# Optimization experiments

Hardware: AMD Instinct MI355X
Metric: run time of the kernel (lower is better)

Reference implementation:

```python
import jax, jax.numpy as jnp
import numpy as np

DIM = 512
NUM_HEADS = 8
HEAD_DIM = DIM // NUM_HEADS
B, N = 2, 4096


def setup_inputs() -> dict:
    key = jax.random.key(0)
    k1, k2, k3, k4, k5 = jax.random.split(key, 5)
    s = 1.0 / np.sqrt(DIM)
    return {
        "x": jax.random.normal(k1, (B, N, DIM), dtype=jnp.float32),
        "w_qkv": jax.random.normal(k2, (DIM, 3 * DIM), dtype=jnp.float32) * s,
        "b_qkv": jax.random.normal(k3, (3 * DIM,), dtype=jnp.float32) * 0.01,
        "w_proj": jax.random.normal(k4, (DIM, DIM), dtype=jnp.float32) * s,
        "b_proj": jax.random.normal(k5, (DIM,), dtype=jnp.float32) * 0.01,
    }


def reference(x, w_qkv, b_qkv, w_proj, b_proj):
    b, n, c = x.shape
    h, d = NUM_HEADS, HEAD_DIM
    qkv = x @ w_qkv + b_qkv                      # [B,N,3C]
    q, k, v = jnp.split(qkv, 3, axis=-1)
    # [B,N,C] -> [B,H,N,D]
    q = q.reshape(b, n, h, d).transpose(0, 2, 1, 3)
    k = k.reshape(b, n, h, d).transpose(0, 2, 1, 3)
    v = v.reshape(b, n, h, d).transpose(0, 2, 1, 3)
    scale = d ** (-0.5)
    attn = jnp.einsum('bhqd,bhkd->bhqk', q, k) * scale  # [B,H,N,N]
    attn = jax.nn.softmax(attn, axis=-1)
    out = jnp.einsum('bhqk,bhkd->bhqd', attn, v)        # [B,H,N,D]
    out = out.transpose(0, 2, 1, 3).reshape(b, n, c)
    return out @ w_proj + b_proj
```

## Files before the change

### kernel.cpp

```cpp
#include <hip/hip_runtime.h>

#define DIM_C 512
#define HEADS 8
#define HD 64
#define BATCH 2
#define SEQ 4096
#define QSCALE (0.125f * 1.44269504088896f)

typedef __attribute__((ext_vector_type(8))) short short8;
typedef __attribute__((ext_vector_type(4))) float f32x4;

__device__ __forceinline__ ushort f2bf(float f) {
    union { float f; unsigned u; } x; x.f = f;
    unsigned r = x.u + 0x7fffu + ((x.u >> 16) & 1u);
    return (ushort)(r >> 16);
}

__device__ __forceinline__ void gl_lds16(const void* g, void* l) {
    __builtin_amdgcn_global_load_lds(
        (const __attribute__((address_space(1))) unsigned int*)g,
        (__attribute__((address_space(3))) unsigned int*)l, 16, 0, 0);
}

__device__ __forceinline__ unsigned cvt_pk_bf16(float lo, float hi) {
    unsigned w;
    asm("v_cvt_pk_bf16_f32 %0, %1, %2" : "=v"(w) : "v"(lo), "v"(hi));
    return w;
}

__global__ __launch_bounds__(256)
void convert_bf16(const float* __restrict__ in, ushort* __restrict__ out, int n4) {
    int i = blockIdx.x * blockDim.x + threadIdx.x;
    const int stride = gridDim.x * blockDim.x;
    for (; i < n4; i += stride) {
        const float4 v = reinterpret_cast<const float4*>(in)[i];
        ushort4 o;
        o.x = f2bf(v.x); o.y = f2bf(v.y); o.z = f2bf(v.z); o.w = f2bf(v.w);
        reinterpret_cast<ushort4*>(out)[i] = o;
    }
}

__global__ __launch_bounds__(256)
void transpose_w_bf16(const float* __restrict__ in, ushort* __restrict__ out,
                      int R, int C) {
    __shared__ ushort Ls[64 * 68];
    const int tid = threadIdx.x;
    const int c0 = blockIdx.x * 64, r0 = blockIdx.y * 64;
    #pragma unroll
    for (int p = 0; p < 4; ++p) {
        const int idx = tid + p * 256;
        const int r = idx >> 4, c4 = (idx & 15) * 4;
        const float4 v = *reinterpret_cast<const float4*>(
            &in[(size_t)(r0 + r) * C + c0 + c4]);
        ushort4 o; o.x = f2bf(v.x); o.y = f2bf(v.y); o.z = f2bf(v.z); o.w = f2bf(v.w);
        *reinterpret_cast<ushort4*>(&Ls[r * 68 + c4]) = o;
    }
    __syncthreads();
    #pragma unroll
    for (int p = 0; p < 4; ++p) {
        const int idx = tid + p * 256;
        const int c = idx >> 4, r4 = (idx & 15) * 4;
        ushort4 o;
        o.x = Ls[(r4 + 0) * 68 + c]; o.y = Ls[(r4 + 1) * 68 + c];
        o.z = Ls[(r4 + 2) * 68 + c]; o.w = Ls[(r4 + 3) * 68 + c];
        *reinterpret_cast<ushort4*>(&out[(size_t)(c0 + c) * R + r0 + r4]) = o;
    }
}

__global__ __launch_bounds__(256)
void transpose_v(const ushort* __restrict__ qkvb, ushort* __restrict__ vt) {
    __shared__ ushort Ls[64 * 68];
    const int tid = threadIdx.x;
    const int n0 = blockIdx.x * 64;
    const int bh = blockIdx.y, b = bh >> 3, h = bh & 7;
    #pragma unroll
    for (int p = 0; p < 4; ++p) {
        const int idx = tid + p * 256;
        const int r = idx >> 4, c4 = (idx & 15) * 4;
        const ushort4 v = *reinterpret_cast<const ushort4*>(
            &qkvb[(size_t)(b * SEQ + n0 + r) * 1536 + 1024 + h * 64 + c4]);
        *reinterpret_cast<ushort4*>(&Ls[r * 68 + c4]) = v;
    }
    __syncthreads();
    #pragma unroll
    for (int p = 0; p < 4; ++p) {
        const int idx = tid + p * 256;
        const int d = idx >> 4, n4 = (idx & 15) * 4;
        ushort4 o;
        o.x = Ls[(n4 + 0) * 68 + d]; o.y = Ls[(n4 + 1) * 68 + d];
        o.z = Ls[(n4 + 2) * 68 + d]; o.w = Ls[(n4 + 3) * 68 + d];
        *reinterpret_cast<ushort4*>(&vt[((size_t)bh * 64 + d) * SEQ + n0 + n4]) = o;
    }
}

template<int MODE>
__global__ __launch_bounds__(256)
void gemm_mfma(const ushort* __restrict__ A, const ushort* __restrict__ BT,
               const float* __restrict__ bias, void* __restrict__ Cout,
               int M, int N, int K) {
    __shared__ ushort As[128 * 64];
    __shared__ ushort Bs[128 * 64];
    const int tid = threadIdx.x;
    const int lane = tid & 63, wid = tid >> 6;
    const int lr = lane & 15, lg = lane >> 4;
    const int wm = wid >> 1, wn = wid & 1;
    const int rowBase = blockIdx.y * 128, colBase = blockIdx.x * 128;
    const int l8 = lane >> 3;
    const int lchunk = (lane & 7) ^ l8;

    f32x4 acc[4][4];
    #pragma unroll
    for (int i = 0; i < 4; ++i)
        #pragma unroll
        for (int j = 0; j < 4; ++j)
            #pragma unroll
            for (int c = 0; c < 4; ++c) acc[i][j][c] = 0.f;

    for (int k0 = 0; k0 < K; k0 += 64) {
        #pragma unroll
        for (int i = 0; i < 4; ++i) {
            const int r = wid * 32 + i * 8;
            gl_lds16(&A[(size_t)(rowBase + r + l8) * K + k0 + lchunk * 8],
                     &As[r * 64]);
            gl_lds16(&BT[(size_t)(colBase + r + l8) * K + k0 + lchunk * 8],
                     &Bs[r * 64]);
        }
        __syncthreads();
        #pragma unroll
        for (int s = 0; s < 2; ++s) {
            short8 af[4], bf[4];
            #pragma unroll
            for (int mt = 0; mt < 4; ++mt) {
                const int r = wm * 64 + mt * 16 + lr;
                af[mt] = *reinterpret_cast<const short8*>(
                    &As[r * 64 + ((s * 4 + lg) ^ (r & 7)) * 8]);
            }
            #pragma unroll
            for (int nt = 0; nt < 4; ++nt) {
                const int r = wn * 64 + nt * 16 + lr;
                bf[nt] = *reinterpret_cast<const short8*>(
                    &Bs[r * 64 + ((s * 4 + lg) ^ (r & 7)) * 8]);
            }
            #pragma unroll
            for (int mt = 0; mt < 4; ++mt)
                #pragma unroll
                for (int nt = 0; nt < 4; ++nt)
                    acc[mt][nt] = __builtin_amdgcn_mfma_f32_16x16x32_bf16(
                        bf[nt], af[mt], acc[mt][nt], 0, 0, 0);
        }
        __syncthreads();
    }

    #pragma unroll
    for (int nt = 0; nt < 4; ++nt) {
        const int c0 = colBase + wn * 64 + nt * 16 + lg * 4;
        const float4 bv = *reinterpret_cast<const float4*>(&bias[c0]);
        const float qs = (MODE == 1 && c0 < DIM_C) ? QSCALE : 1.f;
        #pragma unroll
        for (int mt = 0; mt < 4; ++mt) {
            const int row = rowBase + wm * 64 + mt * 16 + lr;
            if (MODE == 0) {
                float4 o;
                o.x = acc[mt][nt][0] + bv.x; o.y = acc[mt][nt][1] + bv.y;
                o.z = acc[mt][nt][2] + bv.z; o.w = acc[mt][nt][3] + bv.w;
                *reinterpret_cast<float4*>(
                    &reinterpret_cast<float*>(Cout)[(size_t)row * N + c0]) = o;
            } else {
                uint2 o;
                o.x = cvt_pk_bf16((acc[mt][nt][0] + bv.x) * qs,
                                  (acc[mt][nt][1] + bv.y) * qs);
                o.y = cvt_pk_bf16((acc[mt][nt][2] + bv.z) * qs,
                                  (acc[mt][nt][3] + bv.w) * qs);
                *reinterpret_cast<uint2*>(
                    &reinterpret_cast<ushort*>(Cout)[(size_t)row * N + c0]) = o;
            }
        }
    }
}

__global__ __launch_bounds__(512)
void flash_attn7(const ushort* __restrict__ qkvb, const ushort* __restrict__ vt,
                 ushort* __restrict__ aoutb) {
    __shared__ ushort Ks[2][64 * 64];
    __shared__ ushort Vs[2][64 * 64];
    __shared__ ushort Ps[8 * 16 * 64];

    const int tid = threadIdx.x;
    const int lane = tid & 63, wid = tid >> 6;
    const int lr = lane & 15, lg = lane >> 4;
    const int qt = blockIdx.x, bh = blockIdx.y;
    const int b = bh >> 3, h = bh & 7;
    const int q0 = qt * 128;
    const int l8 = lane >> 3;
    const int lchunk = (lane & 7) ^ l8;
    const int rsw = (lr & 7) ^ ((lr >> 3) << 2);

    short8 onesf;
    #pragma unroll
    for (int i = 0; i < 8; ++i) onesf[i] = (short)0x3F80;

    short8 qf[2];
    {
        const size_t qrow = (size_t)b * SEQ + q0 + wid * 16 + lr;
        #pragma unroll
        for (int s = 0; s < 2; ++s)
            qf[s] = *reinterpret_cast<const short8*>(
                &qkvb[qrow * 1536 + h * 64 + s * 32 + lg * 8]);
    }

    float m = -1e30f;
    f32x4 lacc;
    lacc[0] = 0.f; lacc[1] = 0.f; lacc[2] = 0.f; lacc[3] = 0.f;
    f32x4 oa[4];
    #pragma unroll
    for (int dt = 0; dt < 4; ++dt)
        #pragma unroll
        for (int c = 0; c < 4; ++c) oa[dt][c] = 0.f;

    auto stage = [&](int kt, int buf) {
        const int k0 = kt * 64;
        const int r = wid * 8;
        gl_lds16(&qkvb[(size_t)(b * SEQ + k0 + r + l8) * 1536 + DIM_C +
                       h * 64 + lchunk * 8],
                 &Ks[buf][r * 64]);
        gl_lds16(&vt[((size_t)bh * 64 + r + l8) * SEQ + k0 + lchunk * 8],
                 &Vs[buf][r * 64]);
    };

    stage(0, 0);
    const int NT = SEQ / 64;
    for (int kt = 0; kt < NT; ++kt) {
        const int buf = kt & 1;
        __syncthreads();
        if (kt + 1 < NT) stage(kt + 1, buf ^ 1);

        f32x4 sa[4];
        #pragma unroll
        for (int t = 0; t < 4; ++t)
            #pragma unroll
            for (int c = 0; c < 4; ++c) sa[t][c] = 0.f;
        __builtin_amdgcn_s_setprio(1);
        #pragma unroll
        for (int t = 0; t < 4; ++t) {
            const int n = t * 16 + lr;
            #pragma unroll
            for (int s = 0; s < 2; ++s) {
                const short8 kf = *reinterpret_cast<const short8*>(
                    &Ks[buf][n * 64 + ((s * 4 + lg) ^ (n & 7)) * 8]);
                sa[t] = __builtin_amdgcn_mfma_f32_16x16x32_bf16(
                    kf, qf[s], sa[t], 0, 0, 0);
            }
        }
        __builtin_amdgcn_s_setprio(0);

        float mx = fmaxf(fmaxf(sa[0][0], sa[0][1]), sa[0][2]);
        mx = fmaxf(fmaxf(mx, sa[0][3]), sa[1][0]);
        mx = fmaxf(fmaxf(mx, sa[1][1]), sa[1][2]);
        mx = fmaxf(fmaxf(mx, sa[1][3]), sa[2][0]);
        mx = fmaxf(fmaxf(mx, sa[2][1]), sa[2][2]);
        mx = fmaxf(fmaxf(mx, sa[2][3]), sa[3][0]);
        mx = fmaxf(fmaxf(mx, sa[3][1]), sa[3][2]);
        mx = fmaxf(mx, sa[3][3]);
        mx = fmaxf(mx, __shfl_xor(mx, 16));
        mx = fmaxf(mx, __shfl_xor(mx, 32));
        if (__any(mx > m + 8.f)) {
            const float mnew = fmaxf(m, mx);
            const float alpha = exp2f(m - mnew);
            m = mnew;
            lacc[0] *= alpha; lacc[1] *= alpha;
            lacc[2] *= alpha; lacc[3] *= alpha;
            const float a0 = __shfl(alpha, lg * 4 + 0);
            const float a1 = __shfl(alpha, lg * 4 + 1);
            const float a2 = __shfl(alpha, lg * 4 + 2);
            const float a3 = __shfl(alpha, lg * 4 + 3);
            #pragma unroll
            for (int dt = 0; dt < 4; ++dt) {
                oa[dt][0] *= a0; oa[dt][1] *= a1;
                oa[dt][2] *= a2; oa[dt][3] *= a3;
            }
        }
        #pragma unroll
        for (int t = 0; t < 4; ++t)
            #pragma unroll
            for (int r = 0; r < 4; ++r)
                sa[t][r] = exp2f(sa[t][r] - m);

        const int pb = wid * (16 * 64);
        const int pbase = pb + lr * 64 + (lg & 1) * 4;
        #pragma unroll
        for (int t = 0; t < 4; ++t) {
            const int chunk = (2 * t + (lg >> 1)) ^ rsw;
            uint2 w;
            w.x = cvt_pk_bf16(sa[t][0], sa[t][1]);
            w.y = cvt_pk_bf16(sa[t][2], sa[t][3]);
            *reinterpret_cast<uint2*>(&Ps[pbase + chunk * 8]) = w;
        }

        short8 pf[2];
        #pragma unroll
        for (int s = 0; s < 2; ++s)
            pf[s] = *reinterpret_cast<const short8*>(
                &Ps[pb + lr * 64 + ((lg + 4 * s) ^ rsw) * 8]);

        __builtin_amdgcn_s_setprio(1);
        #pragma unroll
        for (int s = 0; s < 2; ++s)
            lacc = __builtin_amdgcn_mfma_f32_16x16x32_bf16(
                onesf, pf[s], lacc, 0, 0, 0);
        #pragma unroll
        for (int dt = 0; dt < 4; ++dt) {
            const int d = dt * 16 + lr;
            #pragma unroll
            for (int s = 0; s < 2; ++s) {
                const short8 vf = *reinterpret_cast<const short8*>(
                    &Vs[buf][d * 64 + ((s * 4 + lg) ^ (d & 7)) * 8]);
                oa[dt] = __builtin_amdgcn_mfma_f32_16x16x32_bf16(
                    pf[s], vf, oa[dt], 0, 0, 0);
            }
        }
        __builtin_amdgcn_s_setprio(0);
    }

    const float linv = 1.f / lacc[0];
    const float v0 = __shfl(linv, lg * 4 + 0);
    const float v1 = __shfl(linv, lg * 4 + 1);
    const float v2 = __shfl(linv, lg * 4 + 2);
    const float v3 = __shfl(linv, lg * 4 + 3);
    const size_t orow0 = (size_t)b * SEQ + q0 + wid * 16;
    #pragma unroll
    for (int dt = 0; dt < 4; ++dt) {
        const int c = h * HD + dt * 16 + lr;
        aoutb[(orow0 + lg * 4 + 0) * DIM_C + c] = f2bf(oa[dt][0] * v0);
        aoutb[(orow0 + lg * 4 + 1) * DIM_C + c] = f2bf(oa[dt][1] * v1);
        aoutb[(orow0 + lg * 4 + 2) * DIM_C + c] = f2bf(oa[dt][2] * v2);
        aoutb[(orow0 + lg * 4 + 3) * DIM_C + c] = f2bf(oa[dt][3] * v3);
    }
}

extern "C" void kernel_launch(void* const* d_in, const int* in_sizes, int n_in,
                              void* d_out, int out_size, void* d_ws, size_t ws_size,
                              hipStream_t stream) {
    const float* x      = (const float*)d_in[0];
    const float* w_qkv  = (const float*)d_in[1];
    const float* b_qkv  = (const float*)d_in[2];
    const float* w_proj = (const float*)d_in[3];
    const float* b_proj = (const float*)d_in[4];
    float* out = (float*)d_out;

    const int M = BATCH * SEQ;
    ushort* xb     = (ushort*)d_ws;
    ushort* wqkvT  = xb     + (size_t)M * DIM_C;
    ushort* wprojT = wqkvT  + (size_t)3 * DIM_C * DIM_C;
    ushort* qkvb   = wprojT + (size_t)DIM_C * DIM_C;
    ushort* vt     = qkvb   + (size_t)M * 3 * DIM_C;
    ushort* aoutb  = vt     + (size_t)16 * HD * SEQ;

    convert_bf16<<<2048, 256, 0, stream>>>(x, xb, M * DIM_C / 4);
    transpose_w_bf16<<<dim3(3 * DIM_C / 64, DIM_C / 64), 256, 0, stream>>>(
        w_qkv, wqkvT, DIM_C, 3 * DIM_C);
    transpose_w_bf16<<<dim3(DIM_C / 64, DIM_C / 64), 256, 0, stream>>>(
        w_proj, wprojT, DIM_C, DIM_C);

    gemm_mfma<1><<<dim3(3 * DIM_C / 128, M / 128), 256, 0, stream>>>(
        xb, wqkvT, b_qkv, qkvb, M, 3 * DIM_C, DIM_C);

    transpose_v<<<dim3(SEQ / 64, BATCH * HEADS), 256, 0, stream>>>(qkvb, vt);

    flash_attn7<<<dim3(SEQ / 128, BATCH * HEADS), 512, 0, stream>>>(
        qkvb, vt, aoutb);

    gemm_mfma<0><<<dim3(DIM_C / 128, M / 128), 256, 0, stream>>>(
        aoutb, wprojT, b_proj, out, M, DIM_C, DIM_C);
}
```

Baseline: 251.2 us.

## Double attention key tile to 128 and switch GEMM epilogue to scalar stores

The flash-attention kernel now stages 128 keys per iteration instead of 64. It computes eight score tiles per step and processes the P·V product in two 64-key halves, which halves the loop trip count, barriers and online-softmax max checks. The GEMM swaps its MFMA operand order so the accumulator layout changes, and its epilogue now writes per-element scalar stores with a scalar bias load instead of vector float4/uint2 stores. The larger tile raises LDS use and register pressure, and the scalar epilogue may coalesce worse than the vector stores.

After: 243.0 us. 3.3% less time.

```diff
diff --git a/kernel.cpp b/kernel.cpp
--- a/kernel.cpp
+++ b/kernel.cpp
@@ -146,43 +146,36 @@
                 #pragma unroll
                 for (int nt = 0; nt < 4; ++nt)
                     acc[mt][nt] = __builtin_amdgcn_mfma_f32_16x16x32_bf16(
-                        bf[nt], af[mt], acc[mt][nt], 0, 0, 0);
+                        af[mt], bf[nt], acc[mt][nt], 0, 0, 0);
         }
         __syncthreads();
     }
 
     #pragma unroll
     for (int nt = 0; nt < 4; ++nt) {
-        const int c0 = colBase + wn * 64 + nt * 16 + lg * 4;
-        const float4 bv = *reinterpret_cast<const float4*>(&bias[c0]);
-        const float qs = (MODE == 1 && c0 < DIM_C) ? QSCALE : 1.f;
+        const int col = colBase + wn * 64 + nt * 16 + lr;
+        const float bv = bias[col];
+        const float qs = (MODE == 1 && col < DIM_C) ? QSCALE : 1.f;
         #pragma unroll
         for (int mt = 0; mt < 4; ++mt) {
-            const int row = rowBase + wm * 64 + mt * 16 + lr;
-            if (MODE == 0) {
-                float4 o;
-                o.x = acc[mt][nt][0] + bv.x; o.y = acc[mt][nt][1] + bv.y;
-                o.z = acc[mt][nt][2] + bv.z; o.w = acc[mt][nt][3] + bv.w;
-                *reinterpret_cast<float4*>(
-                    &reinterpret_cast<float*>(Cout)[(size_t)row * N + c0]) = o;
-            } else {
-                uint2 o;
-                o.x = cvt_pk_bf16((acc[mt][nt][0] + bv.x) * qs,
-                                  (acc[mt][nt][1] + bv.y) * qs);
-                o.y = cvt_pk_bf16((acc[mt][nt][2] + bv.z) * qs,
-                                  (acc[mt][nt][3] + bv.w) * qs);
-                *reinterpret_cast<uint2*>(
-                    &reinterpret_cast<ushort*>(Cout)[(size_t)row * N + c0]) = o;
+            #pragma unroll
+            for (int j = 0; j < 4; ++j) {
+                const int row = rowBase + wm * 64 + mt * 16 + lg * 4 + j;
+                const float v = (acc[mt][nt][j] + bv) * qs;
+                if (MODE == 0)
+                    reinterpret_cast<float*>(Cout)[(size_t)row * N + col] = v;
+                else
+                    reinterpret_cast<ushort*>(Cout)[(size_t)row * N + col] = f2bf(v);
             }
         }
     }
 }
 
 __global__ __launch_bounds__(512)
-void flash_attn7(const ushort* __restrict__ qkvb, const ushort* __restrict__ vt,
+void flash_attn8(const ushort* __restrict__ qkvb, const ushort* __restrict__ vt,
                  ushort* __restrict__ aoutb) {
-    __shared__ ushort Ks[2][64 * 64];
-    __shared__ ushort Vs[2][64 * 64];
+    __shared__ ushort Ks[2][128 * 64];
+    __shared__ ushort Vs[2][64 * 128];
     __shared__ ushort Ps[8 * 16 * 64];
 
     const int tid = threadIdx.x;
@@ -218,30 +211,40 @@
         for (int c = 0; c < 4; ++c) oa[dt][c] = 0.f;
 
     auto stage = [&](int kt, int buf) {
-        const int k0 = kt * 64;
-        const int r = wid * 8;
-        gl_lds16(&qkvb[(size_t)(b * SEQ + k0 + r + l8) * 1536 + DIM_C +
-                       h * 64 + lchunk * 8],
-                 &Ks[buf][r * 64]);
-        gl_lds16(&vt[((size_t)bh * 64 + r + l8) * SEQ + k0 + lchunk * 8],
-                 &Vs[buf][r * 64]);
+        const int k0 = kt * 128;
+        #pragma unroll
+        for (int i = 0; i < 2; ++i) {
+            const int r = wid * 16 + i * 8;
+            gl_lds16(&qkvb[(size_t)(b * SEQ + k0 + r + l8) * 1536 + DIM_C +
+                           h * 64 + lchunk * 8],
+                     &Ks[buf][r * 64]);
+        }
+        #pragma unroll
+        for (int i = 0; i < 2; ++i) {
+            const int d0 = wid * 8 + i * 4;
+            const int d = d0 + (lane >> 4);
+            const int c16 = lane & 15;
+            const int gch = (c16 & 8) | ((c16 & 7) ^ (d & 7));
+            gl_lds16(&vt[((size_t)bh * 64 + d) * SEQ + k0 + gch * 8],
+                     &Vs[buf][d0 * 128]);
+        }
     };
 
     stage(0, 0);
-    const int NT = SEQ / 64;
+    const int NT = SEQ / 128;
     for (int kt = 0; kt < NT; ++kt) {
         const int buf = kt & 1;
         __syncthreads();
         if (kt + 1 < NT) stage(kt + 1, buf ^ 1);
 
-        f32x4 sa[4];
-        #pragma unroll
-        for (int t = 0; t < 4; ++t)
+        f32x4 sa[8];
+        #pragma unroll
+        for (int t = 0; t < 8; ++t)
             #pragma unroll
             for (int c = 0; c < 4; ++c) sa[t][c] = 0.f;
         __builtin_amdgcn_s_setprio(1);
         #pragma unroll
-        for (int t = 0; t < 4; ++t) {
+        for (int t = 0; t < 8; ++t) {
             const int n = t * 16 + lr;
             #pragma unroll
             for (int s = 0; s < 2; ++s) {
@@ -254,13 +257,11 @@
         __builtin_amdgcn_s_setprio(0);
 
         float mx = fmaxf(fmaxf(sa[0][0], sa[0][1]), sa[0][2]);
-        mx = fmaxf(fmaxf(mx, sa[0][3]), sa[1][0]);
-        mx = fmaxf(fmaxf(mx, sa[1][1]), sa[1][2]);
-        mx = fmaxf(fmaxf(mx, sa[1][3]), sa[2][0]);
-        mx = fmaxf(fmaxf(mx, sa[2][1]), sa[2][2]);
-        mx = fmaxf(fmaxf(mx, sa[2][3]), sa[3][0]);
-        mx = fmaxf(fmaxf(mx, sa[3][1]), sa[3][2]);
-        mx = fmaxf(mx, sa[3][3]);
+        #pragma unroll
+        for (int t = 1; t < 8; ++t)
+            mx = fmaxf(fmaxf(mx, sa[t][0]),
+                       fmaxf(fmaxf(sa[t][1], sa[t][2]), sa[t][3]));
+        mx = fmaxf(mx, sa[0][3]);
         mx = fmaxf(mx, __shfl_xor(mx, 16));
         mx = fmaxf(mx, __shfl_xor(mx, 32));
         if (__any(mx > m + 8.f)) {
@@ -280,7 +281,7 @@
             }
         }
         #pragma unroll
-        for (int t = 0; t < 4; ++t)
+        for (int t = 0; t < 8; ++t)
             #pragma unroll
             for (int r = 0; r < 4; ++r)
                 sa[t][r] = exp2f(sa[t][r] - m);
@@ -288,37 +289,40 @@
         const int pb = wid * (16 * 64);
         const int pbase = pb + lr * 64 + (lg & 1) * 4;
         #pragma unroll
-        for (int t = 0; t < 4; ++t) {
-            const int chunk = (2 * t + (lg >> 1)) ^ rsw;
-            uint2 w;
-            w.x = cvt_pk_bf16(sa[t][0], sa[t][1]);
-            w.y = cvt_pk_bf16(sa[t][2], sa[t][3]);
-            *reinterpret_cast<uint2*>(&Ps[pbase + chunk * 8]) = w;
-        }
-
-        short8 pf[2];
-        #pragma unroll
-        for (int s = 0; s < 2; ++s)
-            pf[s] = *reinterpret_cast<const short8*>(
-                &Ps[pb + lr * 64 + ((lg + 4 * s) ^ rsw) * 8]);
-
-        __builtin_amdgcn_s_setprio(1);
-        #pragma unroll
-        for (int s = 0; s < 2; ++s)
-            lacc = __builtin_amdgcn_mfma_f32_16x16x32_bf16(
-                onesf, pf[s], lacc, 0, 0, 0);
-        #pragma unroll
-        for (int dt = 0; dt < 4; ++dt) {
-            const int d = dt * 16 + lr;
-            #pragma unroll
-            for (int s = 0; s < 2; ++s) {
-                const short8 vf = *reinterpret_cast<const short8*>(
-                    &Vs[buf][d * 64 + ((s * 4 + lg) ^ (d & 7)) * 8]);
-                oa[dt] = __builtin_amdgcn_mfma_f32_16x16x32_bf16(
-                    pf[s], vf, oa[dt], 0, 0, 0);
-            }
-        }
-        __builtin_amdgcn_s_setprio(0);
+        for (int kh = 0; kh < 2; ++kh) {
+            #pragma unroll
+            for (int t = 0; t < 4; ++t) {
+                const int chunk = (2 * t + (lg >> 1)) ^ rsw;
+                uint2 w;
+                w.x = cvt_pk_bf16(sa[kh * 4 + t][0], sa[kh * 4 + t][1]);
+                w.y = cvt_pk_bf16(sa[kh * 4 + t][2], sa[kh * 4 + t][3]);
+                *reinterpret_cast<uint2*>(&Ps[pbase + chunk * 8]) = w;
+            }
+            short8 pf[2];
+            #pragma unroll
+            for (int s = 0; s < 2; ++s)
+                pf[s] = *reinterpret_cast<const short8*>(
+                    &Ps[pb + lr * 64 + ((lg + 4 * s) ^ rsw) * 8]);
+
+            __builtin_amdgcn_s_setprio(1);
+            #pragma unroll
+            for (int s = 0; s < 2; ++s)
+                lacc = __builtin_amdgcn_mfma_f32_16x16x32_bf16(
+                    onesf, pf[s], lacc, 0, 0, 0);
+            #pragma unroll
+            for (int dt = 0; dt < 4; ++dt) {
+                const int d = dt * 16 + lr;
+                #pragma unroll
+                for (int s = 0; s < 2; ++s) {
+                    const short8 vf = *reinterpret_cast<const short8*>(
+                        &Vs[buf][d * 128 +
+                                 (kh * 8 + ((s * 4 + lg) ^ (d & 7))) * 8]);
+                    oa[dt] = __builtin_amdgcn_mfma_f32_16x16x32_bf16(
+                        pf[s], vf, oa[dt], 0, 0, 0);
+                }
+            }
+            __builtin_amdgcn_s_setprio(0);
+        }
     }
 
     const float linv = 1.f / lacc[0];
@@ -366,7 +370,7 @@
 
     transpose_v<<<dim3(SEQ / 64, BATCH * HEADS), 256, 0, stream>>>(qkvb, vt);
 
-    flash_attn7<<<dim3(SEQ / 128, BATCH * HEADS), 512, 0, stream>>>(
+    flash_attn8<<<dim3(SEQ / 128, BATCH * HEADS), 512, 0, stream>>>(
         qkvb, vt, aoutb);
 
     gemm_mfma<0><<<dim3(DIM_C / 128, M / 128), 256, 0, stream>>>(
```
